# Performance work log

Measured on AMD Instinct MI355X. Metric: run time of the kernel, lower is better.

Reference implementation:

```python
import jax, jax.numpy as jnp
import numpy as np

SLOPE = 0.01  # torch LeakyReLU default negative_slope

def lrelu(x):
    return jax.nn.leaky_relu(x, SLOPE)

def rgcn_conv(x, edge_index, edge_type, rel_w, root_w, bias, num_relations=2):
    # PyG RGCNConv: out = x @ root + bias + sum_r mean_{edges of rel r into i}(x_j @ W_r)
    N = x.shape[0]
    src, dst = edge_index[0], edge_index[1]
    out = x @ root_w + bias
    # transform once per relation at node level, then gather per edge
    h = jnp.einsum('nd,rde->rne', x, rel_w)          # [R, N, d]
    msg = h[edge_type, src]                           # [E, d] single gather
    for r in range(num_relations):
        m = (edge_type == r)
        s = jax.ops.segment_sum(jnp.where(m[:, None], msg, 0.0), dst, num_segments=N)
        cnt = jax.ops.segment_sum(m.astype(x.dtype), dst, num_segments=N)
        out = out + s / jnp.maximum(cnt, 1.0)[:, None]  # mean aggregation (0 if no edges)
    return out


def setup_inputs() -> dict:
    key = jax.random.key(0)
    ks = jax.random.split(key, 24)
    N, E, H = 50000, 800000, 256
    Q = H // 4
    def lin(k, i, o):
        k1, k2 = jax.random.split(k)
        s = 1.0 / np.sqrt(i)
        return (jax.random.uniform(k1, (i, o), jnp.float32, -s, s),
                jax.random.uniform(k2, (o,), jnp.float32, -s, s))
    Wd, bd = lin(ks[0], 768, Q)
    Wt, bt = lin(ks[1], 768, Q)
    Wn, bn = lin(ks[2], 5, Q)
    Wc, bc = lin(ks[3], 3, Q)
    Wi, bi = lin(ks[4], H, H)
    Wo1, bo1 = lin(ks[5], H, H)
    Wo2, bo2 = lin(ks[6], H, 2)
    s = 1.0 / np.sqrt(H)
    rel_w1 = jax.random.uniform(ks[7], (2, H, H), jnp.float32, -s, s)
    root_w1 = jax.random.uniform(ks[8], (H, H), jnp.float32, -s, s)
    bias1 = jnp.zeros((H,), jnp.float32)
    rel_w2 = jax.random.uniform(ks[9], (2, H, H), jnp.float32, -s, s)
    root_w2 = jax.random.uniform(ks[10], (H, H), jnp.float32, -s, s)
    bias2 = jnp.zeros((H,), jnp.float32)
    return {
        'des': jax.random.normal(ks[11], (N, 768), jnp.float32),
        'tweet': jax.random.normal(ks[12], (N, 768), jnp.float32),
        'num_prop': jax.random.normal(ks[13], (N, 5), jnp.float32),
        'cat_prop': jax.random.normal(ks[14], (N, 3), jnp.float32),
        'edge_index': jax.random.randint(ks[15], (2, E), 0, N, jnp.int32),
        'edge_type': jax.random.randint(ks[16], (E,), 0, 2, jnp.int32),
        'Wd': Wd, 'bd': bd, 'Wt': Wt, 'bt': bt, 'Wn': Wn, 'bn': bn, 'Wc': Wc, 'bc': bc,
        'Wi': Wi, 'bi': bi,
        'rel_w1': rel_w1, 'root_w1': root_w1, 'bias1': bias1,
        'rel_w2': rel_w2, 'root_w2': root_w2, 'bias2': bias2,
        'Wo1': Wo1, 'bo1': bo1, 'Wo2': Wo2, 'bo2': bo2,
    }


def reference(des, tweet, num_prop, cat_prop, edge_index, edge_type,
              Wd, bd, Wt, bt, Wn, bn, Wc, bc, Wi, bi,
              rel_w1, root_w1, bias1, rel_w2, root_w2, bias2,
              Wo1, bo1, Wo2, bo2):
    # dropout is identity in eval mode
    d = lrelu(des @ Wd + bd)
    t = lrelu(tweet @ Wt + bt)
    n = lrelu(num_prop @ Wn + bn)
    c = lrelu(cat_prop @ Wc + bc)
    x = jnp.concatenate([d, t, n, c], axis=1)           # [N, H]
    x = lrelu(x @ Wi + bi)
    x = rgcn_conv(x, edge_index, edge_type, rel_w1, root_w1, bias1)
    x = rgcn_conv(x, edge_index, edge_type, rel_w2, root_w2, bias2)
    x = lrelu(x @ Wo1 + bo1)
    return x @ Wo2 + bo2                                 # [N, 2]
```

## Files before the change

kernel.cpp:

```cpp
#include <hip/hip_runtime.h>
#include <stdint.h>

__device__ __forceinline__ float bf2f(unsigned short h) {
    union { unsigned int u; float f; } x;
    x.u = ((unsigned int)h) << 16;
    return x.f;
}
__device__ __forceinline__ unsigned short f2bf(float f) {
    union { float f; unsigned int u; } x;
    x.f = f;
    unsigned int u = x.u;
    unsigned int r = (u + 0x7FFFu + ((u >> 16) & 1u)) >> 16;
    return (unsigned short)r;
}
__device__ __forceinline__ unsigned pk2(float a, float b) {
    unsigned ua = __float_as_uint(a) + 0x8000u;
    unsigned ub = __float_as_uint(b) + 0x8000u;
    return __builtin_amdgcn_perm(ub, ua, 0x07060302);
}

typedef __attribute__((ext_vector_type(8))) short short8;
typedef __attribute__((ext_vector_type(4))) float floatx4;

__global__ __launch_bounds__(256) void k_encode(
    const float* __restrict__ Ades, const float* __restrict__ Atw,
    const unsigned short* __restrict__ BtDes, const unsigned short* __restrict__ BtTw,
    const unsigned short* __restrict__ bias_bf,
    unsigned short* __restrict__ C, int M)
{
    __shared__ __align__(16) unsigned short Asw[64 * 64];
    __shared__ __align__(16) unsigned short Bsw[64 * 64];

    const int set = blockIdx.y;
    const float* A = set ? Atw : Ades;
    const unsigned short* Bt = set ? BtTw : BtDes;
    const unsigned short* bias = bias_bf + set * 64;
    const int colofs = set * 64;
    const int tid  = threadIdx.x;
    const int wv   = tid >> 6, lane = tid & 63;
    const int quad = lane >> 4, l16 = lane & 15;
    const int m0   = blockIdx.x * 64;

    const int ar  = tid >> 4;
    const int af4 = tid & 15;
    const int bcol = tid >> 3;
    const int bq   = tid & 7;

    floatx4 acc[4];
#pragma unroll
    for (int j = 0; j < 4; j++) acc[j] = (floatx4){0.f, 0.f, 0.f, 0.f};

    for (int kt = 0; kt < 768; kt += 64) {
        if (kt) __syncthreads();
#pragma unroll
        for (int p = 0; p < 4; p++) {
            int row = p * 16 + ar;
            int gr = m0 + row; if (gr > M - 1) gr = M - 1;
            float4 v = *(const float4*)(A + (size_t)gr * 768 + kt + af4 * 4);
            unsigned w0 = pk2(v.x, v.y), w1 = pk2(v.z, v.w);
            int qd = (af4 >> 1) ^ (row & 7);
            uint2 u; u.x = w0; u.y = w1;
            *(uint2*)&Asw[row * 64 + qd * 8 + (af4 & 1) * 4] = u;
        }
#pragma unroll
        for (int p = 0; p < 2; p++) {
            int col = p * 32 + bcol;
            short8 bv = *(const short8*)(Bt + (size_t)col * 768 + kt + bq * 8);
            int qd = bq ^ (col & 7);
            *(short8*)&Bsw[col * 64 + qd * 8] = bv;
        }
        __syncthreads();
#pragma unroll
        for (int s = 0; s < 2; s++) {
            int arow = wv * 16 + l16;
            int ca = (s * 4 + quad) ^ (arow & 7);
            short8 av = *(const short8*)&Asw[arow * 64 + ca * 8];
#pragma unroll
            for (int j = 0; j < 4; j++) {
                int bcl = j * 16 + l16;
                int cb = (s * 4 + quad) ^ (bcl & 7);
                short8 bvr = *(const short8*)&Bsw[bcl * 64 + cb * 8];
                acc[j] = __builtin_amdgcn_mfma_f32_16x16x32_bf16(av, bvr, acc[j], 0, 0, 0);
            }
        }
    }

#pragma unroll
    for (int j = 0; j < 4; j++) {
        float bv = bf2f(bias[j * 16 + l16]);
#pragma unroll
        for (int r = 0; r < 4; r++) {
            int gr = m0 + wv * 16 + quad * 4 + r;
            if (gr < M) {
                float v = acc[j][r] + bv;
                v = v > 0.f ? v : 0.01f * v;
                C[(size_t)gr * 256 + colofs + j * 16 + l16] = f2bf(v);
            }
        }
    }
}

__global__ __launch_bounds__(256) void gemm_nt(
    const unsigned short* __restrict__ A0, const unsigned short* __restrict__ A1,
    const unsigned short* __restrict__ A2, int lda,
    const unsigned short* __restrict__ Bt, int ldb,
    unsigned short* __restrict__ C, int ldc,
    const unsigned short* __restrict__ bias,
    int M, int K, int act)
{
    constexpr int BM = 128, BN = 128, BK = 64;
    const int tid  = threadIdx.x;
    const int wave = tid >> 6;
    const int lane = tid & 63;
    const int quad = lane >> 4;
    const int l16  = lane & 15;
    const int m0   = blockIdx.x * BM;
    const int n0   = blockIdx.y * BN;
    const int wm   = (wave & 1) * 64;
    const int wn   = (wave >> 1) * 64;

    __shared__ short8 As[8 * (BM + 2)];
    __shared__ short8 Bs[8 * (BN + 2)];

    floatx4 acc[4][4];
#pragma unroll
    for (int i = 0; i < 4; i++)
#pragma unroll
        for (int j = 0; j < 4; j++) acc[i][j] = (floatx4){0.f, 0.f, 0.f, 0.f};

    for (int kt = 0; kt < K; kt += BK) {
        const unsigned short* Ap = (kt < 256) ? A0 : (kt < 512) ? A1 : A2;
        const int ko = kt & 255;
#pragma unroll
        for (int c = 0; c < 4; c++) {
            int lin = c * 256 + tid;
            int row = lin >> 3, kq = lin & 7;
            int gr = m0 + row; if (gr > M - 1) gr = M - 1;
            As[kq * (BM + 2) + row] = *(const short8*)(Ap + (size_t)gr * lda + ko + kq * 8);
        }
#pragma unroll
        for (int c = 0; c < 4; c++) {
            int lin = c * 256 + tid;
            int n = lin >> 3, kq = lin & 7;
            Bs[kq * (BN + 2) + n] = *(const short8*)(Bt + (size_t)(n0 + n) * ldb + kt + kq * 8);
        }
        __syncthreads();
#pragma unroll
        for (int s = 0; s < 2; s++) {
            short8 af[4], bfr[4];
#pragma unroll
            for (int i = 0; i < 4; i++)
                af[i] = As[(s * 4 + quad) * (BM + 2) + wm + i * 16 + l16];
#pragma unroll
            for (int j = 0; j < 4; j++)
                bfr[j] = Bs[(s * 4 + quad) * (BN + 2) + wn + j * 16 + l16];
#pragma unroll
            for (int i = 0; i < 4; i++)
#pragma unroll
                for (int j = 0; j < 4; j++)
                    acc[i][j] = __builtin_amdgcn_mfma_f32_16x16x32_bf16(
                        af[i], bfr[j], acc[i][j], 0, 0, 0);
        }
        __syncthreads();
    }

#pragma unroll
    for (int j = 0; j < 4; j++) {
        int gc = n0 + wn + j * 16 + l16;
        float bv = bias ? bf2f(bias[gc]) : 0.f;
#pragma unroll
        for (int i = 0; i < 4; i++) {
            int grb = m0 + wm + i * 16 + quad * 4;
#pragma unroll
            for (int r = 0; r < 4; r++) {
                int gr = grb + r;
                if (gr < M) {
                    float v = acc[i][j][r] + bv;
                    if (act) v = v > 0.f ? v : 0.01f * v;
                    C[(size_t)gr * ldc + gc] = f2bf(v);
                }
            }
        }
    }
}

__global__ void k_prep(const float* __restrict__ Wd, const float* __restrict__ Wt,
                       const float* __restrict__ Wi, const float* __restrict__ Wo1,
                       const float* __restrict__ root1, const float* __restrict__ rel1,
                       const float* __restrict__ root2, const float* __restrict__ rel2,
                       const float* __restrict__ bd, const float* __restrict__ bt,
                       const float* __restrict__ bi, const float* __restrict__ b1,
                       const float* __restrict__ b2, const float* __restrict__ bo1,
                       unsigned short* __restrict__ WdT, unsigned short* __restrict__ WtT,
                       unsigned short* __restrict__ WiT, unsigned short* __restrict__ Wo1T,
                       unsigned short* __restrict__ BT1, unsigned short* __restrict__ BT2,
                       unsigned short* __restrict__ bias_bf)
{
    int i = blockIdx.x * 256 + threadIdx.x;
    if (i < 49152) { int r = i >> 6, c = i & 63; WdT[c * 768 + r] = f2bf(Wd[i]); return; }
    i -= 49152;
    if (i < 49152) { int r = i >> 6, c = i & 63; WtT[c * 768 + r] = f2bf(Wt[i]); return; }
    i -= 49152;
    if (i < 65536) { int r = i >> 8, c = i & 255; WiT[c * 256 + r] = f2bf(Wi[i]); return; }
    i -= 65536;
    if (i < 65536) { int r = i >> 8, c = i & 255; Wo1T[c * 256 + r] = f2bf(Wo1[i]); return; }
    i -= 65536;
    if (i < 196608) {
        int k = i % 768, n = i / 768;
        BT1[i] = f2bf(k < 256 ? root1[k * 256 + n] : rel1[(k - 256) * 256 + n]);
        return;
    }
    i -= 196608;
    if (i < 196608) {
        int k = i % 768, n = i / 768;
        BT2[i] = f2bf(k < 256 ? root2[k * 256 + n] : rel2[(k - 256) * 256 + n]);
        return;
    }
    i -= 196608;
    if (i < 1152) {
        const float* p; int off;
        if (i < 64)       { p = bd;  off = i; }
        else if (i < 128) { p = bt;  off = i - 64; }
        else if (i < 384) { p = bi;  off = i - 128; }
        else if (i < 640) { p = b1;  off = i - 384; }
        else if (i < 896) { p = b2;  off = i - 640; }
        else              { p = bo1; off = i - 896; }
        bias_bf[i] = f2bf(p[off]);
    }
}

__global__ void k_hist(const int* __restrict__ ei, const int* __restrict__ et,
                       int* cnt2, int N, int E) {
    int e = blockIdx.x * 256 + threadIdx.x;
    if (e < E) {
        int dst = ei[E + e];
        int t = et[e] & 1;
        if ((unsigned)dst < (unsigned)N) atomicAdd(&cnt2[t * N + dst], 1);
    }
}

__global__ void k_scan1(const int* __restrict__ cnt2, int* rowptr, int* bsum, int N) {
    __shared__ int sh[256];
    int t = threadIdx.x;
    int base = blockIdx.x * 1024 + t * 4;
    int v[4];
    int s = 0;
#pragma unroll
    for (int k = 0; k < 4; k++) {
        int idx = base + k;
        v[k] = (idx < N) ? (cnt2[idx] + cnt2[N + idx]) : 0;
        s += v[k];
    }
    sh[t] = s;
    __syncthreads();
    for (int off = 1; off < 256; off <<= 1) {
        int x = 0;
        if (t >= off) x = sh[t - off];
        __syncthreads();
        if (t >= off) sh[t] += x;
        __syncthreads();
    }
    int excl = sh[t] - s;
    int run = excl;
#pragma unroll
    for (int k = 0; k < 4; k++) {
        int idx = base + k;
        if (idx < N) rowptr[idx] = run;
        run += v[k];
    }
    if (t == 255) bsum[blockIdx.x] = sh[255];
}

__global__ void k_scan2(const int* __restrict__ bsum, int* bofs, int nb) {
    int t = threadIdx.x;
    int v = (t < nb) ? bsum[t] : 0;
    int orig = v;
    for (int off = 1; off < 64; off <<= 1) {
        int x = __shfl_up(v, off);
        if (t >= off) v += x;
    }
    if (t < nb) bofs[t] = v - orig;
}

__global__ void k_scan3(int* rowptr, const int* __restrict__ bofs, int N) {
    int i = blockIdx.x * 256 + threadIdx.x;
    if (i < N) rowptr[i] += bofs[i >> 10];
}

__global__ void k_fill(const int* __restrict__ ei, const int* __restrict__ et,
                       const int* __restrict__ rowptr, int* cursor, int* sorted,
                       int N, int E) {
    int e = blockIdx.x * 256 + threadIdx.x;
    if (e < E) {
        int src = ei[e];
        int dst = ei[E + e];
        int t = et[e] & 1;
        if ((unsigned)dst < (unsigned)N && (unsigned)src < (unsigned)N) {
            int pos = rowptr[dst] + atomicAdd(&cursor[dst], 1);
            sorted[pos] = src | (t << 24);
        }
    }
}

__global__ __launch_bounds__(256) void k_agg(
    const unsigned short* __restrict__ x,
    unsigned short* __restrict__ m0,
    unsigned short* __restrict__ m1,
    int N,
    const int* __restrict__ rowptr, const int* __restrict__ cnt2,
    const int* __restrict__ sorted)
{
    int wave = threadIdx.x >> 6;
    int lane = threadIdx.x & 63;
    int half = lane >> 5;
    int l32  = lane & 31;
    int node = blockIdx.x * 4 + wave;
    if (node >= N) return;

    int start = rowptr[node];
    int c0 = cnt2[node], c1 = cnt2[N + node];
    int deg = c0 + c1;

    float a0[8] = {0,0,0,0,0,0,0,0};
    float a1[8] = {0,0,0,0,0,0,0,0};

    for (int b = 0; b < deg; b += 64) {
        int rem = deg - b; if (rem > 64) rem = 64;
        int p = 0;
        if (lane < rem) p = sorted[start + b + lane];
        int iters = (rem + 1) >> 1;
        for (int t = 0; t < iters; t += 2) {
            int e0 = 2 * t + half;
            int e1 = e0 + 2;
            int q0 = __shfl(p, e0 < 64 ? e0 : 63);
            int q1 = __shfl(p, e1 < 64 ? e1 : 63);
            bool v0ok = e0 < rem;
            bool v1ok = e1 < rem;
            int s0 = q0 & 0xFFFFFF; if (s0 >= N) s0 = 0;
            int s1 = q1 & 0xFFFFFF; if (s1 >= N) s1 = 0;
            uint4 r0 = *((const uint4*)(x + (size_t)s0 * 256) + l32);
            uint4 r1 = *((const uint4*)(x + (size_t)s1 * 256) + l32);
            if (v0ok) {
                float f[8];
                f[0] = bf2f((unsigned short)(r0.x & 0xFFFFu)); f[1] = bf2f((unsigned short)(r0.x >> 16));
                f[2] = bf2f((unsigned short)(r0.y & 0xFFFFu)); f[3] = bf2f((unsigned short)(r0.y >> 16));
                f[4] = bf2f((unsigned short)(r0.z & 0xFFFFu)); f[5] = bf2f((unsigned short)(r0.z >> 16));
                f[6] = bf2f((unsigned short)(r0.w & 0xFFFFu)); f[7] = bf2f((unsigned short)(r0.w >> 16));
                if ((q0 >> 24) & 1) {
#pragma unroll
                    for (int k = 0; k < 8; k++) a1[k] += f[k];
                } else {
#pragma unroll
                    for (int k = 0; k < 8; k++) a0[k] += f[k];
                }
            }
            if (v1ok) {
                float f[8];
                f[0] = bf2f((unsigned short)(r1.x & 0xFFFFu)); f[1] = bf2f((unsigned short)(r1.x >> 16));
                f[2] = bf2f((unsigned short)(r1.y & 0xFFFFu)); f[3] = bf2f((unsigned short)(r1.y >> 16));
                f[4] = bf2f((unsigned short)(r1.z & 0xFFFFu)); f[5] = bf2f((unsigned short)(r1.z >> 16));
                f[6] = bf2f((unsigned short)(r1.w & 0xFFFFu)); f[7] = bf2f((unsigned short)(r1.w >> 16));
                if ((q1 >> 24) & 1) {
#pragma unroll
                    for (int k = 0; k < 8; k++) a1[k] += f[k];
                } else {
#pragma unroll
                    for (int k = 0; k < 8; k++) a0[k] += f[k];
                }
            }
        }
    }
#pragma unroll
    for (int k = 0; k < 8; k++) {
        a0[k] += __shfl_xor(a0[k], 32);
        a1[k] += __shfl_xor(a1[k], 32);
    }
    float i0 = c0 > 0 ? 1.f / (float)c0 : 0.f;
    float i1 = c1 > 0 ? 1.f / (float)c1 : 0.f;
    uint4 o;
    if (half == 0) {
        o.x = (unsigned)f2bf(a0[0] * i0) | ((unsigned)f2bf(a0[1] * i0) << 16);
        o.y = (unsigned)f2bf(a0[2] * i0) | ((unsigned)f2bf(a0[3] * i0) << 16);
        o.z = (unsigned)f2bf(a0[4] * i0) | ((unsigned)f2bf(a0[5] * i0) << 16);
        o.w = (unsigned)f2bf(a0[6] * i0) | ((unsigned)f2bf(a0[7] * i0) << 16);
        *((uint4*)(m0 + (size_t)node * 256) + l32) = o;
    } else {
        o.x = (unsigned)f2bf(a1[0] * i1) | ((unsigned)f2bf(a1[1] * i1) << 16);
        o.y = (unsigned)f2bf(a1[2] * i1) | ((unsigned)f2bf(a1[3] * i1) << 16);
        o.z = (unsigned)f2bf(a1[4] * i1) | ((unsigned)f2bf(a1[5] * i1) << 16);
        o.w = (unsigned)f2bf(a1[6] * i1) | ((unsigned)f2bf(a1[7] * i1) << 16);
        *((uint4*)(m1 + (size_t)node * 256) + l32) = o;
    }
}

__global__ void k_small(const float* __restrict__ num, const float* __restrict__ cat,
                        const float* __restrict__ Wn, const float* __restrict__ bnp,
                        const float* __restrict__ Wc, const float* __restrict__ bcp,
                        unsigned short* __restrict__ xcat, int N)
{
    __shared__ float wn[320], wc[192], bns[64], bcs[64];
    int t = threadIdx.x;
    for (int i = t; i < 320; i += 256) wn[i] = Wn[i];
    for (int i = t; i < 192; i += 256) wc[i] = Wc[i];
    if (t < 64) { bns[t] = bnp[t]; bcs[t] = bcp[t]; }
    __syncthreads();

    int node = blockIdx.x * 128 + (t >> 1);
    int half = t & 1;
    if (node >= N) return;
    if (half == 0) {
        float in5[5];
#pragma unroll
        for (int i = 0; i < 5; i++) in5[i] = num[(size_t)node * 5 + i];
        unsigned short* orow = xcat + (size_t)node * 256 + 128;
#pragma unroll 4
        for (int c = 0; c < 64; c++) {
            float v = bns[c];
#pragma unroll
            for (int i = 0; i < 5; i++) v += in5[i] * wn[i * 64 + c];
            v = v > 0.f ? v : 0.01f * v;
            orow[c] = f2bf(v);
        }
    } else {
        float in3[3];
#pragma unroll
        for (int i = 0; i < 3; i++) in3[i] = cat[(size_t)node * 3 + i];
        unsigned short* orow = xcat + (size_t)node * 256 + 192;
#pragma unroll 4
        for (int c = 0; c < 64; c++) {
            float v = bcs[c];
#pragma unroll
            for (int i = 0; i < 3; i++) v += in3[i] * wc[i * 64 + c];
            v = v > 0.f ? v : 0.01f * v;
            orow[c] = f2bf(v);
        }
    }
}

__global__ __launch_bounds__(256) void k_final(
    const unsigned short* __restrict__ z,
    const float* __restrict__ Wo2, const float* __restrict__ bo2,
    float* __restrict__ out, int N)
{
    __shared__ float w[512];
    int t = threadIdx.x;
    for (int i = t; i < 512; i += 256) w[i] = Wo2[i];
    __syncthreads();
    int wave = t >> 6, lane = t & 63;
    int node = blockIdx.x * 4 + wave;
    if (node >= N) return;
    uint2 raw = *((const uint2*)(z + (size_t)node * 256) + lane);
    float v0 = bf2f((unsigned short)(raw.x & 0xFFFFu));
    float v1 = bf2f((unsigned short)(raw.x >> 16));
    float v2 = bf2f((unsigned short)(raw.y & 0xFFFFu));
    float v3 = bf2f((unsigned short)(raw.y >> 16));
    int k0 = lane * 4;
    float s0 = v0 * w[k0 * 2]     + v1 * w[(k0 + 1) * 2]     + v2 * w[(k0 + 2) * 2]     + v3 * w[(k0 + 3) * 2];
    float s1 = v0 * w[k0 * 2 + 1] + v1 * w[(k0 + 1) * 2 + 1] + v2 * w[(k0 + 2) * 2 + 1] + v3 * w[(k0 + 3) * 2 + 1];
    for (int off = 32; off; off >>= 1) {
        s0 += __shfl_xor(s0, off);
        s1 += __shfl_xor(s1, off);
    }
    if (lane == 0) {
        out[(size_t)node * 2]     = s0 + bo2[0];
        out[(size_t)node * 2 + 1] = s1 + bo2[1];
    }
}

extern "C" void kernel_launch(void* const* d_in, const int* in_sizes, int n_in,
                              void* d_out, int out_size, void* d_ws, size_t ws_size,
                              hipStream_t stream)
{
    (void)n_in; (void)out_size; (void)ws_size;
    const float* des   = (const float*)d_in[0];
    const float* tweet = (const float*)d_in[1];
    const float* nump  = (const float*)d_in[2];
    const float* catp  = (const float*)d_in[3];
    const int*   ei    = (const int*)d_in[4];
    const int*   et    = (const int*)d_in[5];
    const float* Wd  = (const float*)d_in[6];
    const float* bd  = (const float*)d_in[7];
    const float* Wt  = (const float*)d_in[8];
    const float* bt  = (const float*)d_in[9];
    const float* Wn  = (const float*)d_in[10];
    const float* bn  = (const float*)d_in[11];
    const float* Wc  = (const float*)d_in[12];
    const float* bc  = (const float*)d_in[13];
    const float* Wi  = (const float*)d_in[14];
    const float* bi  = (const float*)d_in[15];
    const float* rel1  = (const float*)d_in[16];
    const float* root1 = (const float*)d_in[17];
    const float* bias1 = (const float*)d_in[18];
    const float* rel2  = (const float*)d_in[19];
    const float* root2 = (const float*)d_in[20];
    const float* bias2 = (const float*)d_in[21];
    const float* Wo1 = (const float*)d_in[22];
    const float* bo1 = (const float*)d_in[23];
    const float* Wo2 = (const float*)d_in[24];
    const float* bo2 = (const float*)d_in[25];

    const int N = in_sizes[0] / 768;
    const int E = in_sizes[5];

    char* ws = (char*)d_ws;
    size_t off = 0;
    auto alloc = [&](size_t bytes) -> char* {
        char* p = ws + off;
        off += (bytes + 255) & ~(size_t)255;
        return p;
    };
    unsigned short* B0 = (unsigned short*)alloc((size_t)N * 256 * 2);
    unsigned short* B1 = (unsigned short*)alloc((size_t)N * 256 * 2);
    unsigned short* B2 = (unsigned short*)alloc((size_t)N * 256 * 2);
    unsigned short* B3 = (unsigned short*)alloc((size_t)N * 256 * 2);
    unsigned short* WdT  = (unsigned short*)alloc(64 * 768 * 2);
    unsigned short* WtT  = (unsigned short*)alloc(64 * 768 * 2);
    unsigned short* WiT  = (unsigned short*)alloc(256 * 256 * 2);
    unsigned short* Wo1T = (unsigned short*)alloc(256 * 256 * 2);
    unsigned short* BT1  = (unsigned short*)alloc(256 * 768 * 2);
    unsigned short* BT2  = (unsigned short*)alloc(256 * 768 * 2);
    unsigned short* bias_bf = (unsigned short*)alloc(1152 * 2);
    unsigned short* bd_bf = bias_bf;
    unsigned short* bi_bf = bias_bf + 128;
    unsigned short* b1_bf = bias_bf + 384;
    unsigned short* b2_bf = bias_bf + 640;
    unsigned short* bo1_bf = bias_bf + 896;
    int* cnt2   = (int*)alloc((size_t)2 * N * 4);
    int* cursor = (int*)alloc((size_t)N * 4);
    int* rowptr = (int*)alloc((size_t)(N + 1) * 4);
    int* bsum   = (int*)alloc(64 * 4);
    int* bofs   = (int*)alloc(64 * 4);
    int* sorted = (int*)alloc((size_t)E * 4);

    size_t zlen = (size_t)(((char*)cursor + (size_t)N * 4) - (char*)cnt2);
    hipMemsetAsync(cnt2, 0, zlen, stream);

    k_prep<<<(623744 + 255) / 256, 256, 0, stream>>>(
        Wd, Wt, Wi, Wo1, root1, rel1, root2, rel2,
        bd, bt, bi, bias1, bias2, bo1,
        WdT, WtT, WiT, Wo1T, BT1, BT2, bias_bf);

    int eb = (E + 255) / 256;
    k_hist<<<eb, 256, 0, stream>>>(ei, et, cnt2, N, E);
    int nb = (N + 1023) / 1024;
    k_scan1<<<nb, 256, 0, stream>>>(cnt2, rowptr, bsum, N);
    k_scan2<<<1, 64, 0, stream>>>(bsum, bofs, nb);
    k_scan3<<<(N + 255) / 256, 256, 0, stream>>>(rowptr, bofs, N);
    k_fill<<<eb, 256, 0, stream>>>(ei, et, rowptr, cursor, sorted, N, E);

    dim3 gEnc((N + 63) / 64, 2);
    k_encode<<<gEnc, 256, 0, stream>>>(des, tweet, WdT, WtT, bd_bf, B0, N);
    k_small<<<(N + 127) / 128, 256, 0, stream>>>(nump, catp, Wn, bn, Wc, bc, B0, N);

    dim3 g128((N + 127) / 128, 2);
    gemm_nt<<<g128, 256, 0, stream>>>(B0, B0, B0, 256, WiT, 256, B1, 256, bi_bf, N, 256, 1);

    int ab = (N + 3) / 4;
    k_agg<<<ab, 256, 0, stream>>>(B1, B2, B3, N, rowptr, cnt2, sorted);
    gemm_nt<<<g128, 256, 0, stream>>>(B1, B2, B3, 256, BT1, 768, B0, 256, b1_bf, N, 768, 0);

    k_agg<<<ab, 256, 0, stream>>>(B0, B2, B3, N, rowptr, cnt2, sorted);
    gemm_nt<<<g128, 256, 0, stream>>>(B0, B2, B3, 256, BT2, 768, B1, 256, b2_bf, N, 768, 0);

    gemm_nt<<<g128, 256, 0, stream>>>(B1, B1, B1, 256, Wo1T, 256, B0, 256, bo1_bf, N, 256, 1);

    k_final<<<ab, 256, 0, stream>>>(B0, Wo2, bo2, (float*)d_out, N);
}
```

Baseline: 743.9 us.

## Double-buffer LDS and prefetch tiles in registers in encoder GEMM

Rewrites the k_encode main loop to use two LDS buffers with register prefetch two tiles ahead, so global loads of the next fp32 A and bf16 B tiles overlap MFMA compute on the current tile. The syncthreads calls are replaced by an lgkmcnt wait plus s_barrier, and address offsets are hoisted out of the loop. This doubles LDS use and adds register pressure from the prefetch buffers, which could lower occupancy.

Result: no change. 741.9 us (-0.3%).

```diff
diff --git a/kernel.cpp b/kernel.cpp
--- a/kernel.cpp
+++ b/kernel.cpp
@@ -19,6 +19,11 @@
     return __builtin_amdgcn_perm(ub, ua, 0x07060302);
 }
 
+__device__ __forceinline__ void pipe_barrier() {
+    asm volatile("s_waitcnt lgkmcnt(0)" ::: "memory");
+    __builtin_amdgcn_s_barrier();
+}
+
 typedef __attribute__((ext_vector_type(8))) short short8;
 typedef __attribute__((ext_vector_type(4))) float floatx4;
 
@@ -28,8 +33,8 @@
     const unsigned short* __restrict__ bias_bf,
     unsigned short* __restrict__ C, int M)
 {
-    __shared__ __align__(16) unsigned short Asw[64 * 64];
-    __shared__ __align__(16) unsigned short Bsw[64 * 64];
+    __shared__ __align__(16) unsigned short Asw[2][64 * 64];
+    __shared__ __align__(16) unsigned short Bsw[2][64 * 64];
 
     const int set = blockIdx.y;
     const float* A = set ? Atw : Ades;
@@ -45,45 +50,69 @@
     const int af4 = tid & 15;
     const int bcol = tid >> 3;
     const int bq   = tid & 7;
+    const int awofs = ar * 64 + ((af4 >> 1) ^ (ar & 7)) * 8 + (af4 & 1) * 4;
+    const int bwofs = bcol * 64 + (bq ^ (bcol & 7)) * 8;
+
+    const float* ap[4];
+#pragma unroll
+    for (int p = 0; p < 4; p++) {
+        int gr = m0 + p * 16 + ar; if (gr > M - 1) gr = M - 1;
+        ap[p] = A + (size_t)gr * 768 + af4 * 4;
+    }
+    const unsigned short* bp0 = Bt + (size_t)bcol * 768 + bq * 8;
+    const unsigned short* bp1 = bp0 + 32 * 768;
+
+    float4 ra0[4], ra1[4];
+    short8 rb0[2], rb1[2];
 
     floatx4 acc[4];
 #pragma unroll
     for (int j = 0; j < 4; j++) acc[j] = (floatx4){0.f, 0.f, 0.f, 0.f};
 
-    for (int kt = 0; kt < 768; kt += 64) {
-        if (kt) __syncthreads();
-#pragma unroll
-        for (int p = 0; p < 4; p++) {
-            int row = p * 16 + ar;
-            int gr = m0 + row; if (gr > M - 1) gr = M - 1;
-            float4 v = *(const float4*)(A + (size_t)gr * 768 + kt + af4 * 4);
-            unsigned w0 = pk2(v.x, v.y), w1 = pk2(v.z, v.w);
-            int qd = (af4 >> 1) ^ (row & 7);
-            uint2 u; u.x = w0; u.y = w1;
-            *(uint2*)&Asw[row * 64 + qd * 8 + (af4 & 1) * 4] = u;
-        }
-#pragma unroll
-        for (int p = 0; p < 2; p++) {
-            int col = p * 32 + bcol;
-            short8 bv = *(const short8*)(Bt + (size_t)col * 768 + kt + bq * 8);
-            int qd = bq ^ (col & 7);
-            *(short8*)&Bsw[col * 64 + qd * 8] = bv;
-        }
-        __syncthreads();
-#pragma unroll
-        for (int s = 0; s < 2; s++) {
-            int arow = wv * 16 + l16;
-            int ca = (s * 4 + quad) ^ (arow & 7);
-            short8 av = *(const short8*)&Asw[arow * 64 + ca * 8];
-#pragma unroll
-            for (int j = 0; j < 4; j++) {
-                int bcl = j * 16 + l16;
-                int cb = (s * 4 + quad) ^ (bcl & 7);
-                short8 bvr = *(const short8*)&Bsw[bcl * 64 + cb * 8];
-                acc[j] = __builtin_amdgcn_mfma_f32_16x16x32_bf16(av, bvr, acc[j], 0, 0, 0);
-            }
-        }
-    }
+    const int arow  = wv * 16 + l16;
+    const int abase = arow * 64;
+    const int amask = arow & 7;
+    const int bmask = l16 & 7;
+
+#define LOADT(t, RA, RB) { \
+    _Pragma("unroll") for (int p = 0; p < 4; p++) RA[p] = *(const float4*)(ap[p] + (t) * 64); \
+    RB[0] = *(const short8*)(bp0 + (t) * 64); \
+    RB[1] = *(const short8*)(bp1 + (t) * 64); }
+
+#define WRITET(buf, RA, RB) { \
+    _Pragma("unroll") for (int p = 0; p < 4; p++) { \
+        uint2 u; u.x = pk2(RA[p].x, RA[p].y); u.y = pk2(RA[p].z, RA[p].w); \
+        *(uint2*)&Asw[buf][awofs + p * 1024] = u; } \
+    *(short8*)&Bsw[buf][bwofs] = RB[0]; \
+    *(short8*)&Bsw[buf][bwofs + 2048] = RB[1]; }
+
+#define COMPUTET(buf) { \
+    _Pragma("unroll") for (int s = 0; s < 2; s++) { \
+        short8 av = *(const short8*)&Asw[buf][abase + ((s * 4 + quad) ^ amask) * 8]; \
+        _Pragma("unroll") for (int j = 0; j < 4; j++) { \
+            short8 bv = *(const short8*)&Bsw[buf][(j * 16 + l16) * 64 + ((s * 4 + quad) ^ bmask) * 8]; \
+            acc[j] = __builtin_amdgcn_mfma_f32_16x16x32_bf16(av, bv, acc[j], 0, 0, 0); } } }
+
+    LOADT(0, ra0, rb0);
+    LOADT(1, ra1, rb1);
+    WRITET(0, ra0, rb0);
+    pipe_barrier();
+
+#pragma unroll
+    for (int tt = 0; tt < 6; tt++) {
+        const int t = tt * 2;
+        if (t + 2 < 12) LOADT(t + 2, ra0, rb0);
+        COMPUTET(0);
+        WRITET(1, ra1, rb1);
+        pipe_barrier();
+        if (t + 3 < 12) LOADT(t + 3, ra1, rb1);
+        COMPUTET(1);
+        if (t + 2 < 12) WRITET(0, ra0, rb0);
+        pipe_barrier();
+    }
+#undef LOADT
+#undef WRITET
+#undef COMPUTET
 
 #pragma unroll
     for (int j = 0; j < 4; j++) {
```

## Load encoder A operands directly into registers and stage half of B in LDS

Applied to the files above, without the earlier changes.

The encoder GEMM now has each wave read its fp32 A rows straight from global memory into registers. A three-slot prefetch ring converts them to bf16 MFMA fragments in place, so A no longer goes through a swizzled LDS tile. The B weight matrix is loaded into padded LDS in two halves of 384 K each, giving only two barriers per block instead of one per 64-wide K step. Blocks grow to 512 threads covering 128 rows. The padded 392 stride is meant to limit bank conflicts, but the per-lane A reads are strided, and the larger LDS footprint may reduce occupancy.

Result: slower. 759.4 us (+2.1%).

```diff
diff --git a/kernel.cpp b/kernel.cpp
--- a/kernel.cpp
+++ b/kernel.cpp
@@ -22,14 +22,13 @@
 typedef __attribute__((ext_vector_type(8))) short short8;
 typedef __attribute__((ext_vector_type(4))) float floatx4;
 
-__global__ __launch_bounds__(256) void k_encode(
+__global__ __launch_bounds__(512) void k_encode(
     const float* __restrict__ Ades, const float* __restrict__ Atw,
     const unsigned short* __restrict__ BtDes, const unsigned short* __restrict__ BtTw,
     const unsigned short* __restrict__ bias_bf,
     unsigned short* __restrict__ C, int M)
 {
-    __shared__ __align__(16) unsigned short Asw[64 * 64];
-    __shared__ __align__(16) unsigned short Bsw[64 * 64];
+    __shared__ unsigned short Bs[64 * 392];
 
     const int set = blockIdx.y;
     const float* A = set ? Atw : Ades;
@@ -39,62 +38,63 @@
     const int tid  = threadIdx.x;
     const int wv   = tid >> 6, lane = tid & 63;
     const int quad = lane >> 4, l16 = lane & 15;
-    const int m0   = blockIdx.x * 64;
-
-    const int ar  = tid >> 4;
-    const int af4 = tid & 15;
-    const int bcol = tid >> 3;
-    const int bq   = tid & 7;
+
+    const int row = blockIdx.x * 128 + wv * 16 + l16;
+    int gr = row; if (gr > M - 1) gr = M - 1;
+    const float* a = A + (size_t)gr * 768 + quad * 8;
 
     floatx4 acc[4];
 #pragma unroll
     for (int j = 0; j < 4; j++) acc[j] = (floatx4){0.f, 0.f, 0.f, 0.f};
 
-    for (int kt = 0; kt < 768; kt += 64) {
-        if (kt) __syncthreads();
-#pragma unroll
-        for (int p = 0; p < 4; p++) {
-            int row = p * 16 + ar;
-            int gr = m0 + row; if (gr > M - 1) gr = M - 1;
-            float4 v = *(const float4*)(A + (size_t)gr * 768 + kt + af4 * 4);
-            unsigned w0 = pk2(v.x, v.y), w1 = pk2(v.z, v.w);
-            int qd = (af4 >> 1) ^ (row & 7);
-            uint2 u; u.x = w0; u.y = w1;
-            *(uint2*)&Asw[row * 64 + qd * 8 + (af4 & 1) * 4] = u;
-        }
-#pragma unroll
-        for (int p = 0; p < 2; p++) {
-            int col = p * 32 + bcol;
-            short8 bv = *(const short8*)(Bt + (size_t)col * 768 + kt + bq * 8);
-            int qd = bq ^ (col & 7);
-            *(short8*)&Bsw[col * 64 + qd * 8] = bv;
+#pragma unroll
+    for (int h = 0; h < 2; h++) {
+        if (h) __syncthreads();
+        for (int c = tid; c < 3072; c += 512) {
+            int n = c / 48, kc = c - n * 48;
+            *(uint4*)&Bs[n * 392 + kc * 8] = ((const uint4*)Bt)[n * 96 + h * 48 + kc];
         }
         __syncthreads();
-#pragma unroll
-        for (int s = 0; s < 2; s++) {
-            int arow = wv * 16 + l16;
-            int ca = (s * 4 + quad) ^ (arow & 7);
-            short8 av = *(const short8*)&Asw[arow * 64 + ca * 8];
-#pragma unroll
-            for (int j = 0; j < 4; j++) {
-                int bcl = j * 16 + l16;
-                int cb = (s * 4 + quad) ^ (bcl & 7);
-                short8 bvr = *(const short8*)&Bsw[bcl * 64 + cb * 8];
-                acc[j] = __builtin_amdgcn_mfma_f32_16x16x32_bf16(av, bvr, acc[j], 0, 0, 0);
+
+        const float* ah = a + h * 384;
+        float4 p0[3], p1[3];
+#pragma unroll
+        for (int i = 0; i < 3; i++) {
+            p0[i] = *(const float4*)(ah + i * 32);
+            p1[i] = *(const float4*)(ah + i * 32 + 4);
+        }
+#pragma unroll
+        for (int s = 0; s < 12; s++) {
+            const int slot = s % 3;
+            short8 af;
+            unsigned* u = (unsigned*)&af;
+            u[0] = pk2(p0[slot].x, p0[slot].y);
+            u[1] = pk2(p0[slot].z, p0[slot].w);
+            u[2] = pk2(p1[slot].x, p1[slot].y);
+            u[3] = pk2(p1[slot].z, p1[slot].w);
+            if (s + 3 < 12) {
+                p0[slot] = *(const float4*)(ah + (s + 3) * 32);
+                p1[slot] = *(const float4*)(ah + (s + 3) * 32 + 4);
             }
-        }
-    }
-
-#pragma unroll
-    for (int j = 0; j < 4; j++) {
-        float bv = bf2f(bias[j * 16 + l16]);
+            const int kb = s * 32 + quad * 8;
+#pragma unroll
+            for (int t = 0; t < 4; t++) {
+                short8 bfr = *(const short8*)&Bs[(t * 16 + l16) * 392 + kb];
+                acc[t] = __builtin_amdgcn_mfma_f32_16x16x32_bf16(af, bfr, acc[t], 0, 0, 0);
+            }
+        }
+    }
+
+#pragma unroll
+    for (int t = 0; t < 4; t++) {
+        float bv = bf2f(bias[t * 16 + l16]);
 #pragma unroll
         for (int r = 0; r < 4; r++) {
-            int gr = m0 + wv * 16 + quad * 4 + r;
-            if (gr < M) {
-                float v = acc[j][r] + bv;
+            int orow = blockIdx.x * 128 + wv * 16 + quad * 4 + r;
+            if (orow < M) {
+                float v = acc[t][r] + bv;
                 v = v > 0.f ? v : 0.01f * v;
-                C[(size_t)gr * 256 + colofs + j * 16 + l16] = f2bf(v);
+                C[(size_t)orow * 256 + colofs + t * 16 + l16] = f2bf(v);
             }
         }
     }
@@ -548,8 +548,8 @@
     k_scan3<<<(N + 255) / 256, 256, 0, stream>>>(rowptr, bofs, N);
     k_fill<<<eb, 256, 0, stream>>>(ei, et, rowptr, cursor, sorted, N, E);
 
-    dim3 gEnc((N + 63) / 64, 2);
-    k_encode<<<gEnc, 256, 0, stream>>>(des, tweet, WdT, WtT, bd_bf, B0, N);
+    dim3 gEnc((N + 127) / 128, 2);
+    k_encode<<<gEnc, 512, 0, stream>>>(des, tweet, WdT, WtT, bd_bf, B0, N);
     k_small<<<(N + 127) / 128, 256, 0, stream>>>(nump, catp, Wn, bn, Wc, bc, B0, N);
 
     dim3 g128((N + 127) / 128, 2);
```
